# Kernel optimization log

Hardware: AMD Instinct MI355X
Metric: run time of the kernel (lower is better)

Reference implementation:

```python
import jax, jax.numpy as jnp
import numpy as np

N_CLASS = 100
HIDDEN = 768
BATCH = 512


def setup_inputs() -> dict:
    key = jax.random.key(0)
    kx, ky, km = jax.random.split(key, 3)
    x = jax.random.normal(kx, (BATCH, HIDDEN), dtype=jnp.float32)
    y = jax.random.randint(ky, (BATCH,), 0, N_CLASS, dtype=jnp.int64 if jax.config.jax_enable_x64 else jnp.int32)
    M = jax.random.normal(km, (N_CLASS, HIDDEN, HIDDEN), dtype=jnp.float32) * 0.1
    return {"x": x, "y": y, "M": M}


def _get_sym_M(M):
    # M: [n_class, H, H]
    h = M.shape[-1]
    Mt = jnp.triu(M)
    diag = Mt * jnp.eye(h, dtype=M.dtype)  # keeps only diagonal entries
    # detached ReLU correction: pushes near-zero/negative diagonal up by ~0.001
    Mt = Mt + jax.lax.stop_gradient(jax.nn.relu(-(diag - 0.001)))
    return jnp.einsum('chk,cjk->chj', Mt, Mt)  # Mt @ Mt^T, symmetric PSD


def reference(x, y, M):
    # Faithful to: one_hot(y) broadcast-select of sym_M then batched matvec.
    # Equivalent efficient form: gather selected class matrix, per-sample matvec.
    sym = _get_sym_M(M)            # [n_class, H, H]
    My = sym[y]                    # [B, H, H] gather (irregular access)
    return jnp.einsum('bh,bhk->bk', x, My)  # [B, H]
```

## Files before the change

### kernel.cpp

```cpp
#include <hip/hip_runtime.h>

#define NCLASS 100
#define HID    768
#define BATCH  512
#define SG     8
#define NPAN   12

__device__ __forceinline__ void build_list(const int* __restrict__ y, int c,
                                           int* slist, int* scnt, int t) {
    if (t < 64) {
        int n = 0;
        for (int r = 0; r < BATCH / 64; ++r) {
            const int b = r * 64 + t;
            const bool hit = (y[b] == c);
            const unsigned long long mask = __ballot(hit);
            if (hit) slist[n + __popcll(mask & ((1ull << t) - 1ull))] = b;
            n += __popcll(mask);
        }
        if (t == 0) *scnt = n;
    }
}

__global__ __launch_bounds__(256, 4) void kA(
    const float* __restrict__ x, const int* __restrict__ y,
    const float* __restrict__ M, float* __restrict__ T)
{
    const int c    = blockIdx.x;
    const int g    = (NPAN - 1) - blockIdx.y;
    const int t    = threadIdx.x;
    const int col0 = g * 64;

    __shared__ int   slist[BATCH];
    __shared__ int   scnt;
    __shared__ float xs[SG][HID];
    __shared__ float Xs[SG];
    __shared__ float red[4][16][4][SG + 1];
    __shared__ float dj_lds[64];

    build_list(y, c, slist, &scnt, t);
    __syncthreads();
    const int cnt = scnt;
    if (cnt == 0) return;

    const float* __restrict__ Mc   = M + (size_t)c * HID * HID;
    const float* __restrict__ Mpan = Mc + col0 + (t & 15) * 4;
    const int wv = t >> 6, ln = t & 63;
    const int hg = t >> 4, jq = t & 15;

    if (t < 64) {
        const int jg = col0 + t;
        dj_lds[t] = fmaxf(Mc[(size_t)jg * HID + jg], 1e-3f);
    }

    for (int g0 = 0; g0 < cnt; g0 += SG) {
        const int gs = min(SG, cnt - g0);
        __syncthreads();
        #pragma unroll
        for (int ss = 0; ss < 2; ++ss) {
            const int s = 2 * wv + ss;
            const int b = slist[g0 + (s < gs ? s : 0)];
            const float4* xr = (const float4*)(x + (size_t)b * HID);
            const float4 v0 = xr[ln], v1 = xr[ln + 64], v2 = xr[ln + 128];
            *(float4*)&xs[s][ln * 4]       = v0;
            *(float4*)&xs[s][ln * 4 + 256] = v1;
            *(float4*)&xs[s][ln * 4 + 512] = v2;
            float pX = ((v0.x + v0.y) + (v0.z + v0.w))
                     + ((v1.x + v1.y) + (v1.z + v1.w))
                     + ((v2.x + v2.y) + (v2.z + v2.w));
            #pragma unroll
            for (int off = 32; off; off >>= 1) pX += __shfl_xor(pX, off);
            if (ln == 0) Xs[s] = pX;
        }
        __syncthreads();

        float tp[4][SG];
        #pragma unroll
        for (int jj = 0; jj < 4; ++jj)
            #pragma unroll
            for (int s = 0; s < SG; ++s) tp[jj][s] = 0.f;

        int hb = 0;
        for (; hb + 128 <= col0; hb += 128) {
            float4 ma[4], mb[4];
            #pragma unroll
            for (int m = 0; m < 4; ++m)
                ma[m] = *(const float4*)(Mpan + (size_t)(hb + hg + 16 * m) * HID);
            #pragma unroll
            for (int m = 0; m < 4; ++m)
                mb[m] = *(const float4*)(Mpan + (size_t)(hb + 64 + hg + 16 * m) * HID);
            #pragma unroll
            for (int m = 0; m < 4; ++m) {
                const int h = hb + hg + 16 * m;
                #pragma unroll
                for (int s = 0; s < SG; ++s) {
                    const float xv = xs[s][h];
                    tp[0][s] = fmaf(xv, ma[m].x, tp[0][s]);
                    tp[1][s] = fmaf(xv, ma[m].y, tp[1][s]);
                    tp[2][s] = fmaf(xv, ma[m].z, tp[2][s]);
                    tp[3][s] = fmaf(xv, ma[m].w, tp[3][s]);
                }
            }
            #pragma unroll
            for (int m = 0; m < 4; ++m) {
                const int h = hb + 64 + hg + 16 * m;
                #pragma unroll
                for (int s = 0; s < SG; ++s) {
                    const float xv = xs[s][h];
                    tp[0][s] = fmaf(xv, mb[m].x, tp[0][s]);
                    tp[1][s] = fmaf(xv, mb[m].y, tp[1][s]);
                    tp[2][s] = fmaf(xv, mb[m].z, tp[2][s]);
                    tp[3][s] = fmaf(xv, mb[m].w, tp[3][s]);
                }
            }
        }
        if (hb < col0) {
            float4 ma[4];
            #pragma unroll
            for (int m = 0; m < 4; ++m)
                ma[m] = *(const float4*)(Mpan + (size_t)(hb + hg + 16 * m) * HID);
            #pragma unroll
            for (int m = 0; m < 4; ++m) {
                const int h = hb + hg + 16 * m;
                #pragma unroll
                for (int s = 0; s < SG; ++s) {
                    const float xv = xs[s][h];
                    tp[0][s] = fmaf(xv, ma[m].x, tp[0][s]);
                    tp[1][s] = fmaf(xv, ma[m].y, tp[1][s]);
                    tp[2][s] = fmaf(xv, ma[m].z, tp[2][s]);
                    tp[3][s] = fmaf(xv, ma[m].w, tp[3][s]);
                }
            }
        }
        {
            float4 ma[4];
            #pragma unroll
            for (int m = 0; m < 4; ++m) {
                const int hrel = hg + 16 * m;
                ma[m] = *(const float4*)(Mpan + (size_t)(col0 + hrel) * HID);
                if (4 * jq + 0 <= hrel) ma[m].x = 0.f;
                if (4 * jq + 1 <= hrel) ma[m].y = 0.f;
                if (4 * jq + 2 <= hrel) ma[m].z = 0.f;
                if (4 * jq + 3 <= hrel) ma[m].w = 0.f;
            }
            #pragma unroll
            for (int m = 0; m < 4; ++m) {
                const int h = col0 + hg + 16 * m;
                #pragma unroll
                for (int s = 0; s < SG; ++s) {
                    const float xv = xs[s][h];
                    tp[0][s] = fmaf(xv, ma[m].x, tp[0][s]);
                    tp[1][s] = fmaf(xv, ma[m].y, tp[1][s]);
                    tp[2][s] = fmaf(xv, ma[m].z, tp[2][s]);
                    tp[3][s] = fmaf(xv, ma[m].w, tp[3][s]);
                }
            }
        }
        #pragma unroll
        for (int m = 16; m <= 32; m <<= 1)
            #pragma unroll
            for (int jj = 0; jj < 4; ++jj)
                #pragma unroll
                for (int s = 0; s < SG; ++s)
                    tp[jj][s] += __shfl_xor(tp[jj][s], m);
        if (ln < 16) {
            #pragma unroll
            for (int jj = 0; jj < 4; ++jj)
                #pragma unroll
                for (int s = 0; s < SG; ++s)
                    red[wv][ln][jj][s] = tp[jj][s];
        }
        __syncthreads();
        {
            const int j = t & 63, jq2 = j >> 2, jj2 = j & 3;
            const int jg = col0 + j;
            #pragma unroll
            for (int ss = 0; ss < 2; ++ss) {
                const int s = (t >> 6) * 2 + ss;
                if (s < gs) {
                    const float u = (red[0][jq2][jj2][s] + red[1][jq2][jj2][s])
                                  + (red[2][jq2][jj2][s] + red[3][jq2][jj2][s]);
                    const float xj = xs[s][jg];
                    T[(size_t)slist[g0 + s] * HID + jg] =
                        u + dj_lds[j] * xj + 1e-3f * (Xs[s] - xj);
                }
            }
        }
    }
}

__global__ __launch_bounds__(256, 4) void kB(
    const int* __restrict__ y, const float* __restrict__ M,
    const float* __restrict__ T, float* __restrict__ out)
{
    const int c  = blockIdx.x;
    const int q  = blockIdx.y;
    const int t  = threadIdx.x;
    const int k0 = q * 64;

    __shared__ int   slist[BATCH];
    __shared__ int   scnt;
    __shared__ float ts[SG][HID];
    __shared__ float Tt[SG];
    __shared__ float ob[SG][64];
    __shared__ float dk_lds[64];

    build_list(y, c, slist, &scnt, t);
    __syncthreads();
    const int cnt = scnt;
    if (cnt == 0) return;

    const float* __restrict__ Mc = M + (size_t)c * HID * HID;
    const int wv = t >> 6, ln = t & 63;
    const int kr = t >> 4, cg = t & 15;
    const float* __restrict__ r0 = Mc + (size_t)(k0 + kr     ) * HID + k0 + cg * 4;
    const float* __restrict__ r1 = Mc + (size_t)(k0 + kr + 16) * HID + k0 + cg * 4;
    const float* __restrict__ r2 = Mc + (size_t)(k0 + kr + 32) * HID + k0 + cg * 4;
    const float* __restrict__ r3 = Mc + (size_t)(k0 + kr + 48) * HID + k0 + cg * 4;

    if (t < 64) {
        const int kg = k0 + t;
        dk_lds[t] = fmaxf(Mc[(size_t)kg * HID + kg], 1e-3f);
    }

    for (int g0 = 0; g0 < cnt; g0 += SG) {
        const int gs = min(SG, cnt - g0);
        __syncthreads();
        #pragma unroll
        for (int ss = 0; ss < 2; ++ss) {
            const int s = 2 * wv + ss;
            const int b = slist[g0 + (s < gs ? s : 0)];
            const float4* tr = (const float4*)(T + (size_t)b * HID);
            const float4 v0 = tr[ln], v1 = tr[ln + 64], v2 = tr[ln + 128];
            *(float4*)&ts[s][ln * 4]       = v0;
            *(float4*)&ts[s][ln * 4 + 256] = v1;
            *(float4*)&ts[s][ln * 4 + 512] = v2;
            float pT = ((v0.x + v0.y) + (v0.z + v0.w))
                     + ((v1.x + v1.y) + (v1.z + v1.w))
                     + ((v2.x + v2.y) + (v2.z + v2.w));
            #pragma unroll
            for (int off = 32; off; off >>= 1) pT += __shfl_xor(pT, off);
            if (ln == 0) Tt[s] = pT;
        }
        __syncthreads();

        float acc[4][SG];
        #pragma unroll
        for (int m = 0; m < 4; ++m)
            #pragma unroll
            for (int s = 0; s < SG; ++s) acc[m][s] = 0.f;

        {
            const int j0 = k0 + cg * 4;
            float4 mq[4];
            mq[0] = *(const float4*)(r0);
            mq[1] = *(const float4*)(r1);
            mq[2] = *(const float4*)(r2);
            mq[3] = *(const float4*)(r3);
            #pragma unroll
            for (int m = 0; m < 4; ++m) {
                const int k = k0 + 16 * m + kr;
                if (j0 + 0 <= k) mq[m].x = 0.f;
                if (j0 + 1 <= k) mq[m].y = 0.f;
                if (j0 + 2 <= k) mq[m].z = 0.f;
                if (j0 + 3 <= k) mq[m].w = 0.f;
            }
            #pragma unroll
            for (int s = 0; s < SG; ++s) {
                const float4 tv = *(const float4*)&ts[s][j0];
                #pragma unroll
                for (int m = 0; m < 4; ++m) {
                    acc[m][s] = fmaf(mq[m].x, tv.x, acc[m][s]);
                    acc[m][s] = fmaf(mq[m].y, tv.y, acc[m][s]);
                    acc[m][s] = fmaf(mq[m].z, tv.z, acc[m][s]);
                    acc[m][s] = fmaf(mq[m].w, tv.w, acc[m][s]);
                }
            }
        }
        int jb = k0 + 64;
        for (; jb + 128 <= HID; jb += 128) {
            float4 ma[4], mb[4];
            ma[0] = *(const float4*)(r0 + (jb - k0));
            ma[1] = *(const float4*)(r1 + (jb - k0));
            ma[2] = *(const float4*)(r2 + (jb - k0));
            ma[3] = *(const float4*)(r3 + (jb - k0));
            mb[0] = *(const float4*)(r0 + (jb - k0) + 64);
            mb[1] = *(const float4*)(r1 + (jb - k0) + 64);
            mb[2] = *(const float4*)(r2 + (jb - k0) + 64);
            mb[3] = *(const float4*)(r3 + (jb - k0) + 64);
            const int j0 = jb + cg * 4;
            #pragma unroll
            for (int s = 0; s < SG; ++s) {
                const float4 tv = *(const float4*)&ts[s][j0];
                #pragma unroll
                for (int m = 0; m < 4; ++m) {
                    acc[m][s] = fmaf(ma[m].x, tv.x, acc[m][s]);
                    acc[m][s] = fmaf(ma[m].y, tv.y, acc[m][s]);
                    acc[m][s] = fmaf(ma[m].z, tv.z, acc[m][s]);
                    acc[m][s] = fmaf(ma[m].w, tv.w, acc[m][s]);
                }
            }
            #pragma unroll
            for (int s = 0; s < SG; ++s) {
                const float4 tv = *(const float4*)&ts[s][j0 + 64];
                #pragma unroll
                for (int m = 0; m < 4; ++m) {
                    acc[m][s] = fmaf(mb[m].x, tv.x, acc[m][s]);
                    acc[m][s] = fmaf(mb[m].y, tv.y, acc[m][s]);
                    acc[m][s] = fmaf(mb[m].z, tv.z, acc[m][s]);
                    acc[m][s] = fmaf(mb[m].w, tv.w, acc[m][s]);
                }
            }
        }
        if (jb < HID) {
            float4 ma[4];
            ma[0] = *(const float4*)(r0 + (jb - k0));
            ma[1] = *(const float4*)(r1 + (jb - k0));
            ma[2] = *(const float4*)(r2 + (jb - k0));
            ma[3] = *(const float4*)(r3 + (jb - k0));
            const int j0 = jb + cg * 4;
            #pragma unroll
            for (int s = 0; s < SG; ++s) {
                const float4 tv = *(const float4*)&ts[s][j0];
                #pragma unroll
                for (int m = 0; m < 4; ++m) {
                    acc[m][s] = fmaf(ma[m].x, tv.x, acc[m][s]);
                    acc[m][s] = fmaf(ma[m].y, tv.y, acc[m][s]);
                    acc[m][s] = fmaf(ma[m].z, tv.z, acc[m][s]);
                    acc[m][s] = fmaf(ma[m].w, tv.w, acc[m][s]);
                }
            }
        }
        #pragma unroll
        for (int m2 = 1; m2 <= 8; m2 <<= 1)
            #pragma unroll
            for (int m = 0; m < 4; ++m)
                #pragma unroll
                for (int s = 0; s < SG; ++s)
                    acc[m][s] += __shfl_xor(acc[m][s], m2);
        if (cg == 0) {
            #pragma unroll
            for (int m = 0; m < 4; ++m)
                #pragma unroll
                for (int s = 0; s < SG; ++s)
                    ob[s][16 * m + kr] = acc[m][s];
        }
        __syncthreads();
        {
            const int j = t & 63;
            const int k = k0 + j;
            #pragma unroll
            for (int ss = 0; ss < 2; ++ss) {
                const int s = (t >> 6) * 2 + ss;
                if (s < gs) {
                    const float tk = ts[s][k];
                    out[(size_t)slist[g0 + s] * HID + k] =
                        ob[s][j] + dk_lds[j] * tk + 1e-3f * (Tt[s] - tk);
                }
            }
        }
    }
}

extern "C" void kernel_launch(void* const* d_in, const int* in_sizes, int n_in,
                              void* d_out, int out_size, void* d_ws, size_t ws_size,
                              hipStream_t stream) {
    const float* x = (const float*)d_in[0];
    const int*   y = (const int*)d_in[1];
    const float* M = (const float*)d_in[2];
    float* out = (float*)d_out;
    float* T   = (float*)d_ws;

    kA<<<dim3(NCLASS, NPAN), 256, 0, stream>>>(x, y, M, T);
    kB<<<dim3(NCLASS, NPAN), 256, 0, stream>>>(y, M, T, out);
}
```

Before: 90.98 us.

## Split triangular panels into balanced row chunks with partial sums and epilogue kernels

Each class's triangular work is split into 24 load-balanced tiles using lookup tables for panel and row-chunk indices, where the old code used 12 uneven column panels. Partial results go to workspace buffers and are combined by two new per-sample epilogue kernels, which also apply the diagonal and epsilon terms. The sample group size is doubled to 16 so each loaded M tile is reused across more samples. This adds two launches, extra workspace traffic and more register pressure, in exchange for better load balance and more parallelism.

```diff
diff --git a/kernel.cpp b/kernel.cpp
--- a/kernel.cpp
+++ b/kernel.cpp
@@ -3,8 +3,13 @@
 #define NCLASS 100
 #define HID    768
 #define BATCH  512
-#define SG     8
-#define NPAN   12
+#define SG     16
+#define BH     (BATCH * HID)
+
+__constant__ int gA_tab[24] = {3,4,5,6,7,7,8,8,9,9,10,10,11,11,11, 2,6,10, 1,5,9, 0,4,8};
+__constant__ int hA_tab[24] = {0,0,0,0,0,1,0,1,0,1, 0, 1, 0, 1, 2, 0,1, 2, 0,1,2, 0,1,2};
+__constant__ int qB_tab[24] = {0,0,1,1,2,2,3,3,4,5,6,7, 0,4,8, 1,5,9, 2,6,10, 3,7,11};
+__constant__ int vB_tab[24] = {1,2,1,2,1,2,1,2,2,2,2,2, 0,1,2, 0,1,2, 0, 1, 2, 0,1, 2};
 
 __device__ __forceinline__ void build_list(const int* __restrict__ y, int c,
                                            int* slist, int* scnt, int t) {
@@ -21,21 +26,22 @@
     }
 }
 
-__global__ __launch_bounds__(256, 4) void kA(
+__global__ __launch_bounds__(256, 3) void kA(
     const float* __restrict__ x, const int* __restrict__ y,
-    const float* __restrict__ M, float* __restrict__ T)
+    const float* __restrict__ M, float* __restrict__ Tp)
 {
+    const int t    = threadIdx.x;
     const int c    = blockIdx.x;
-    const int g    = (NPAN - 1) - blockIdx.y;
-    const int t    = threadIdx.x;
-    const int col0 = g * 64;
+    const int g    = gA_tab[blockIdx.y], h = hA_tab[blockIdx.y];
+    const int col0 = g * 64, row0 = h * 256;
+    const bool hasdiag = (h == (g >> 2));
+    const int rows = min(256, 64 * (g + 1) - row0);
+    const int bulk = hasdiag ? rows - 64 : rows;
 
     __shared__ int   slist[BATCH];
     __shared__ int   scnt;
-    __shared__ float xs[SG][HID];
-    __shared__ float Xs[SG];
+    __shared__ float xs[SG][256];
     __shared__ float red[4][16][4][SG + 1];
-    __shared__ float dj_lds[64];
 
     build_list(y, c, slist, &scnt, t);
     __syncthreads();
@@ -43,33 +49,22 @@
     if (cnt == 0) return;
 
     const float* __restrict__ Mc   = M + (size_t)c * HID * HID;
-    const float* __restrict__ Mpan = Mc + col0 + (t & 15) * 4;
-    const int wv = t >> 6, ln = t & 63;
-    const int hg = t >> 4, jq = t & 15;
-
-    if (t < 64) {
-        const int jg = col0 + t;
-        dj_lds[t] = fmaxf(Mc[(size_t)jg * HID + jg], 1e-3f);
-    }
+    const float* __restrict__ Mpan = Mc + (size_t)row0 * HID + col0 + (t & 15) * 4;
+    const int hg = t >> 4, jq = t & 15, wv = t >> 6, ln = t & 63;
 
     for (int g0 = 0; g0 < cnt; g0 += SG) {
         const int gs = min(SG, cnt - g0);
         __syncthreads();
-        #pragma unroll
-        for (int ss = 0; ss < 2; ++ss) {
-            const int s = 2 * wv + ss;
+        {
+            const int s = t >> 4, l = t & 15;
             const int b = slist[g0 + (s < gs ? s : 0)];
-            const float4* xr = (const float4*)(x + (size_t)b * HID);
-            const float4 v0 = xr[ln], v1 = xr[ln + 64], v2 = xr[ln + 128];
-            *(float4*)&xs[s][ln * 4]       = v0;
-            *(float4*)&xs[s][ln * 4 + 256] = v1;
-            *(float4*)&xs[s][ln * 4 + 512] = v2;
-            float pX = ((v0.x + v0.y) + (v0.z + v0.w))
-                     + ((v1.x + v1.y) + (v1.z + v1.w))
-                     + ((v2.x + v2.y) + (v2.z + v2.w));
-            #pragma unroll
-            for (int off = 32; off; off >>= 1) pX += __shfl_xor(pX, off);
-            if (ln == 0) Xs[s] = pX;
+            const float4* xr = (const float4*)(x + (size_t)b * HID + row0);
+            const float4 v0 = xr[l * 4], v1 = xr[l * 4 + 1],
+                         v2 = xr[l * 4 + 2], v3 = xr[l * 4 + 3];
+            *(float4*)&xs[s][l * 16]      = v0;
+            *(float4*)&xs[s][l * 16 + 4]  = v1;
+            *(float4*)&xs[s][l * 16 + 8]  = v2;
+            *(float4*)&xs[s][l * 16 + 12] = v3;
         }
         __syncthreads();
 
@@ -79,21 +74,21 @@
             #pragma unroll
             for (int s = 0; s < SG; ++s) tp[jj][s] = 0.f;
 
-        int hb = 0;
-        for (; hb + 128 <= col0; hb += 128) {
+        int r = 0;
+        for (; r + 128 <= bulk; r += 128) {
             float4 ma[4], mb[4];
             #pragma unroll
             for (int m = 0; m < 4; ++m)
-                ma[m] = *(const float4*)(Mpan + (size_t)(hb + hg + 16 * m) * HID);
-            #pragma unroll
-            for (int m = 0; m < 4; ++m)
-                mb[m] = *(const float4*)(Mpan + (size_t)(hb + 64 + hg + 16 * m) * HID);
+                ma[m] = *(const float4*)(Mpan + (size_t)(r + hg + 16 * m) * HID);
+            #pragma unroll
+            for (int m = 0; m < 4; ++m)
+                mb[m] = *(const float4*)(Mpan + (size_t)(r + 64 + hg + 16 * m) * HID);
             #pragma unroll
             for (int m = 0; m < 4; ++m) {
-                const int h = hb + hg + 16 * m;
+                const int lr = r + hg + 16 * m;
                 #pragma unroll
                 for (int s = 0; s < SG; ++s) {
-                    const float xv = xs[s][h];
+                    const float xv = xs[s][lr];
                     tp[0][s] = fmaf(xv, ma[m].x, tp[0][s]);
                     tp[1][s] = fmaf(xv, ma[m].y, tp[1][s]);
                     tp[2][s] = fmaf(xv, ma[m].z, tp[2][s]);
@@ -102,10 +97,10 @@
             }
             #pragma unroll
             for (int m = 0; m < 4; ++m) {
-                const int h = hb + 64 + hg + 16 * m;
+                const int lr = r + 64 + hg + 16 * m;
                 #pragma unroll
                 for (int s = 0; s < SG; ++s) {
-                    const float xv = xs[s][h];
+                    const float xv = xs[s][lr];
                     tp[0][s] = fmaf(xv, mb[m].x, tp[0][s]);
                     tp[1][s] = fmaf(xv, mb[m].y, tp[1][s]);
                     tp[2][s] = fmaf(xv, mb[m].z, tp[2][s]);
@@ -113,17 +108,17 @@
                 }
             }
         }
-        if (hb < col0) {
+        if (r < bulk) {
             float4 ma[4];
             #pragma unroll
             for (int m = 0; m < 4; ++m)
-                ma[m] = *(const float4*)(Mpan + (size_t)(hb + hg + 16 * m) * HID);
+                ma[m] = *(const float4*)(Mpan + (size_t)(r + hg + 16 * m) * HID);
             #pragma unroll
             for (int m = 0; m < 4; ++m) {
-                const int h = hb + hg + 16 * m;
+                const int lr = r + hg + 16 * m;
                 #pragma unroll
                 for (int s = 0; s < SG; ++s) {
-                    const float xv = xs[s][h];
+                    const float xv = xs[s][lr];
                     tp[0][s] = fmaf(xv, ma[m].x, tp[0][s]);
                     tp[1][s] = fmaf(xv, ma[m].y, tp[1][s]);
                     tp[2][s] = fmaf(xv, ma[m].z, tp[2][s]);
@@ -131,12 +126,12 @@
                 }
             }
         }
-        {
+        if (hasdiag) {
             float4 ma[4];
             #pragma unroll
             for (int m = 0; m < 4; ++m) {
                 const int hrel = hg + 16 * m;
-                ma[m] = *(const float4*)(Mpan + (size_t)(col0 + hrel) * HID);
+                ma[m] = *(const float4*)(Mpan + (size_t)(bulk + hrel) * HID);
                 if (4 * jq + 0 <= hrel) ma[m].x = 0.f;
                 if (4 * jq + 1 <= hrel) ma[m].y = 0.f;
                 if (4 * jq + 2 <= hrel) ma[m].z = 0.f;
@@ -144,10 +139,10 @@
             }
             #pragma unroll
             for (int m = 0; m < 4; ++m) {
-                const int h = col0 + hg + 16 * m;
+                const int lr = bulk + hg + 16 * m;
                 #pragma unroll
                 for (int s = 0; s < SG; ++s) {
-                    const float xv = xs[s][h];
+                    const float xv = xs[s][lr];
                     tp[0][s] = fmaf(xv, ma[m].x, tp[0][s]);
                     tp[1][s] = fmaf(xv, ma[m].y, tp[1][s]);
                     tp[2][s] = fmaf(xv, ma[m].z, tp[2][s]);
@@ -156,12 +151,12 @@
             }
         }
         #pragma unroll
-        for (int m = 16; m <= 32; m <<= 1)
+        for (int mm = 16; mm <= 32; mm <<= 1)
             #pragma unroll
             for (int jj = 0; jj < 4; ++jj)
                 #pragma unroll
                 for (int s = 0; s < SG; ++s)
-                    tp[jj][s] += __shfl_xor(tp[jj][s], m);
+                    tp[jj][s] += __shfl_xor(tp[jj][s], mm);
         if (ln < 16) {
             #pragma unroll
             for (int jj = 0; jj < 4; ++jj)
@@ -172,37 +167,68 @@
         __syncthreads();
         {
             const int j = t & 63, jq2 = j >> 2, jj2 = j & 3;
-            const int jg = col0 + j;
-            #pragma unroll
-            for (int ss = 0; ss < 2; ++ss) {
-                const int s = (t >> 6) * 2 + ss;
+            #pragma unroll
+            for (int ss = 0; ss < 4; ++ss) {
+                const int s = (t >> 6) * 4 + ss;
                 if (s < gs) {
                     const float u = (red[0][jq2][jj2][s] + red[1][jq2][jj2][s])
                                   + (red[2][jq2][jj2][s] + red[3][jq2][jj2][s]);
-                    const float xj = xs[s][jg];
-                    T[(size_t)slist[g0 + s] * HID + jg] =
-                        u + dj_lds[j] * xj + 1e-3f * (Xs[s] - xj);
+                    Tp[(size_t)h * BH + (size_t)slist[g0 + s] * HID + col0 + j] = u;
                 }
             }
         }
     }
 }
 
-__global__ __launch_bounds__(256, 4) void kB(
+__global__ __launch_bounds__(256) void kT(
+    const float* __restrict__ x, const int* __restrict__ y,
+    const float* __restrict__ M, const float* __restrict__ Tp,
+    float* __restrict__ T)
+{
+    const int b = blockIdx.x, t = threadIdx.x;
+    const int c = y[b];
+    __shared__ float wred[4];
+
+    const float* __restrict__ xb = x + (size_t)b * HID;
+    const float xv0 = xb[t], xv1 = xb[t + 256], xv2 = xb[t + 512];
+    float sx = xv0 + xv1 + xv2;
+    #pragma unroll
+    for (int off = 32; off; off >>= 1) sx += __shfl_xor(sx, off);
+    if ((t & 63) == 0) wred[t >> 6] = sx;
+    __syncthreads();
+    const float X = (wred[0] + wred[1]) + (wred[2] + wred[3]);
+
+    const float* __restrict__ Mc = M + (size_t)c * HID * HID;
+    const size_t bh = (size_t)b * HID;
+    const float u0 = Tp[bh + t];
+    const float u1 = Tp[bh + t + 256] + Tp[BH + bh + t + 256];
+    const float u2 = Tp[bh + t + 512] + Tp[BH + bh + t + 512] + Tp[2 * (size_t)BH + bh + t + 512];
+    const float uu[3] = {u0, u1, u2};
+    const float xx[3] = {xv0, xv1, xv2};
+    #pragma unroll
+    for (int qi = 0; qi < 3; ++qi) {
+        const int j = t + 256 * qi;
+        const float dj = fmaxf(Mc[(size_t)j * (HID + 1)], 1e-3f);
+        T[bh + j] = uu[qi] + dj * xx[qi] + 1e-3f * (X - xx[qi]);
+    }
+}
+
+__global__ __launch_bounds__(256, 3) void kB(
     const int* __restrict__ y, const float* __restrict__ M,
-    const float* __restrict__ T, float* __restrict__ out)
+    const float* __restrict__ T, float* __restrict__ P)
 {
+    const int t  = threadIdx.x;
     const int c  = blockIdx.x;
-    const int q  = blockIdx.y;
-    const int t  = threadIdx.x;
-    const int k0 = q * 64;
+    const int q  = qB_tab[blockIdx.y], v = vB_tab[blockIdx.y];
+    const int k0 = 64 * q;
+    const int c0 = max(256 * v, k0);
+    const int w  = 256 * (v + 1) - c0;
+    const bool hasdiag = (c0 == k0);
 
     __shared__ int   slist[BATCH];
     __shared__ int   scnt;
-    __shared__ float ts[SG][HID];
-    __shared__ float Tt[SG];
-    __shared__ float ob[SG][64];
-    __shared__ float dk_lds[64];
+    __shared__ float ts[SG][256];
+    __shared__ float ob[SG][65];
 
     build_list(y, c, slist, &scnt, t);
     __syncthreads();
@@ -210,36 +236,23 @@
     if (cnt == 0) return;
 
     const float* __restrict__ Mc = M + (size_t)c * HID * HID;
-    const int wv = t >> 6, ln = t & 63;
     const int kr = t >> 4, cg = t & 15;
-    const float* __restrict__ r0 = Mc + (size_t)(k0 + kr     ) * HID + k0 + cg * 4;
-    const float* __restrict__ r1 = Mc + (size_t)(k0 + kr + 16) * HID + k0 + cg * 4;
-    const float* __restrict__ r2 = Mc + (size_t)(k0 + kr + 32) * HID + k0 + cg * 4;
-    const float* __restrict__ r3 = Mc + (size_t)(k0 + kr + 48) * HID + k0 + cg * 4;
-
-    if (t < 64) {
-        const int kg = k0 + t;
-        dk_lds[t] = fmaxf(Mc[(size_t)kg * HID + kg], 1e-3f);
-    }
+    const float* __restrict__ Mrow = Mc + (size_t)(k0 + kr) * HID + c0 + cg * 4;
+    const int jl0 = (c0 - 256 * v) + cg * 4;
 
     for (int g0 = 0; g0 < cnt; g0 += SG) {
         const int gs = min(SG, cnt - g0);
         __syncthreads();
-        #pragma unroll
-        for (int ss = 0; ss < 2; ++ss) {
-            const int s = 2 * wv + ss;
+        {
+            const int s = t >> 4, l = t & 15;
             const int b = slist[g0 + (s < gs ? s : 0)];
-            const float4* tr = (const float4*)(T + (size_t)b * HID);
-            const float4 v0 = tr[ln], v1 = tr[ln + 64], v2 = tr[ln + 128];
-            *(float4*)&ts[s][ln * 4]       = v0;
-            *(float4*)&ts[s][ln * 4 + 256] = v1;
-            *(float4*)&ts[s][ln * 4 + 512] = v2;
-            float pT = ((v0.x + v0.y) + (v0.z + v0.w))
-                     + ((v1.x + v1.y) + (v1.z + v1.w))
-                     + ((v2.x + v2.y) + (v2.z + v2.w));
-            #pragma unroll
-            for (int off = 32; off; off >>= 1) pT += __shfl_xor(pT, off);
-            if (ln == 0) Tt[s] = pT;
+            const float4* tr = (const float4*)(T + (size_t)b * HID + 256 * v);
+            const float4 v0 = tr[l * 4], v1 = tr[l * 4 + 1],
+                         v2 = tr[l * 4 + 2], v3 = tr[l * 4 + 3];
+            *(float4*)&ts[s][l * 16]      = v0;
+            *(float4*)&ts[s][l * 16 + 4]  = v1;
+            *(float4*)&ts[s][l * 16 + 8]  = v2;
+            *(float4*)&ts[s][l * 16 + 12] = v3;
         }
         __syncthreads();
 
@@ -250,23 +263,23 @@
             for (int s = 0; s < SG; ++s) acc[m][s] = 0.f;
 
         {
-            const int j0 = k0 + cg * 4;
             float4 mq[4];
-            mq[0] = *(const float4*)(r0);
-            mq[1] = *(const float4*)(r1);
-            mq[2] = *(const float4*)(r2);
-            mq[3] = *(const float4*)(r3);
-            #pragma unroll
-            for (int m = 0; m < 4; ++m) {
-                const int k = k0 + 16 * m + kr;
-                if (j0 + 0 <= k) mq[m].x = 0.f;
-                if (j0 + 1 <= k) mq[m].y = 0.f;
-                if (j0 + 2 <= k) mq[m].z = 0.f;
-                if (j0 + 3 <= k) mq[m].w = 0.f;
+            #pragma unroll
+            for (int m = 0; m < 4; ++m)
+                mq[m] = *(const float4*)(Mrow + (size_t)(16 * m) * HID);
+            if (hasdiag) {
+                #pragma unroll
+                for (int m = 0; m < 4; ++m) {
+                    const int krel = kr + 16 * m;
+                    if (4 * cg + 0 <= krel) mq[m].x = 0.f;
+                    if (4 * cg + 1 <= krel) mq[m].y = 0.f;
+                    if (4 * cg + 2 <= krel) mq[m].z = 0.f;
+                    if (4 * cg + 3 <= krel) mq[m].w = 0.f;
+                }
             }
             #pragma unroll
             for (int s = 0; s < SG; ++s) {
-                const float4 tv = *(const float4*)&ts[s][j0];
+                const float4 tv = *(const float4*)&ts[s][jl0];
                 #pragma unroll
                 for (int m = 0; m < 4; ++m) {
                     acc[m][s] = fmaf(mq[m].x, tv.x, acc[m][s]);
@@ -276,21 +289,18 @@
                 }
             }
         }
-        int jb = k0 + 64;
-        for (; jb + 128 <= HID; jb += 128) {
+        int cb = 64;
+        for (; cb + 128 <= w; cb += 128) {
             float4 ma[4], mb[4];
-            ma[0] = *(const float4*)(r0 + (jb - k0));
-            ma[1] = *(const float4*)(r1 + (jb - k0));
-            ma[2] = *(const float4*)(r2 + (jb - k0));
-            ma[3] = *(const float4*)(r3 + (jb - k0));
-            mb[0] = *(const float4*)(r0 + (jb - k0) + 64);
-            mb[1] = *(const float4*)(r1 + (jb - k0) + 64);
-            mb[2] = *(const float4*)(r2 + (jb - k0) + 64);
-            mb[3] = *(const float4*)(r3 + (jb - k0) + 64);
-            const int j0 = jb + cg * 4;
+            #pragma unroll
+            for (int m = 0; m < 4; ++m)
+                ma[m] = *(const float4*)(Mrow + (size_t)(16 * m) * HID + cb);
+            #pragma unroll
+            for (int m = 0; m < 4; ++m)
+                mb[m] = *(const float4*)(Mrow + (size_t)(16 * m) * HID + cb + 64);
             #pragma unroll
             for (int s = 0; s < SG; ++s) {
-                const float4 tv = *(const float4*)&ts[s][j0];
+                const float4 tv = *(const float4*)&ts[s][jl0 + cb];
                 #pragma unroll
                 for (int m = 0; m < 4; ++m) {
                     acc[m][s] = fmaf(ma[m].x, tv.x, acc[m][s]);
@@ -301,7 +311,7 @@
             }
             #pragma unroll
             for (int s = 0; s < SG; ++s) {
-                const float4 tv = *(const float4*)&ts[s][j0 + 64];
+                const float4 tv = *(const float4*)&ts[s][jl0 + cb + 64];
                 #pragma unroll
                 for (int m = 0; m < 4; ++m) {
                     acc[m][s] = fmaf(mb[m].x, tv.x, acc[m][s]);
@@ -311,16 +321,14 @@
                 }
             }
         }
-        if (jb < HID) {
+        if (cb < w) {
             float4 ma[4];
-            ma[0] = *(const float4*)(r0 + (jb - k0));
-            ma[1] = *(const float4*)(r1 + (jb - k0));
-            ma[2] = *(const float4*)(r2 + (jb - k0));
-            ma[3] = *(const float4*)(r3 + (jb - k0));
-            const int j0 = jb + cg * 4;
+            #pragma unroll
+            for (int m = 0; m < 4; ++m)
+                ma[m] = *(const float4*)(Mrow + (size_t)(16 * m) * HID + cb);
             #pragma unroll
             for (int s = 0; s < SG; ++s) {
-                const float4 tv = *(const float4*)&ts[s][j0];
+                const float4 tv = *(const float4*)&ts[s][jl0 + cb];
                 #pragma unroll
                 for (int m = 0; m < 4; ++m) {
                     acc[m][s] = fmaf(ma[m].x, tv.x, acc[m][s]);
@@ -331,33 +339,61 @@
             }
         }
         #pragma unroll
-        for (int m2 = 1; m2 <= 8; m2 <<= 1)
+        for (int mm = 1; mm <= 8; mm <<= 1)
             #pragma unroll
             for (int m = 0; m < 4; ++m)
                 #pragma unroll
                 for (int s = 0; s < SG; ++s)
-                    acc[m][s] += __shfl_xor(acc[m][s], m2);
+                    acc[m][s] += __shfl_xor(acc[m][s], mm);
         if (cg == 0) {
             #pragma unroll
             for (int m = 0; m < 4; ++m)
                 #pragma unroll
                 for (int s = 0; s < SG; ++s)
-                    ob[s][16 * m + kr] = acc[m][s];
+                    ob[s][kr + 16 * m] = acc[m][s];
         }
         __syncthreads();
         {
             const int j = t & 63;
-            const int k = k0 + j;
-            #pragma unroll
-            for (int ss = 0; ss < 2; ++ss) {
-                const int s = (t >> 6) * 2 + ss;
-                if (s < gs) {
-                    const float tk = ts[s][k];
-                    out[(size_t)slist[g0 + s] * HID + k] =
-                        ob[s][j] + dk_lds[j] * tk + 1e-3f * (Tt[s] - tk);
-                }
-            }
-        }
+            #pragma unroll
+            for (int ss = 0; ss < 4; ++ss) {
+                const int s = (t >> 6) * 4 + ss;
+                if (s < gs)
+                    P[(size_t)v * BH + (size_t)slist[g0 + s] * HID + k0 + j] = ob[s][j];
+            }
+        }
+    }
+}
+
+__global__ __launch_bounds__(256) void k3(
+    const int* __restrict__ y, const float* __restrict__ M,
+    const float* __restrict__ T, const float* __restrict__ P,
+    float* __restrict__ out)
+{
+    const int b = blockIdx.x, t = threadIdx.x;
+    const int c = y[b];
+    __shared__ float wred[4];
+
+    const size_t bh = (size_t)b * HID;
+    const float t0 = T[bh + t], t1 = T[bh + t + 256], t2 = T[bh + t + 512];
+    float st = t0 + t1 + t2;
+    #pragma unroll
+    for (int off = 32; off; off >>= 1) st += __shfl_xor(st, off);
+    if ((t & 63) == 0) wred[t >> 6] = st;
+    __syncthreads();
+    const float Tt = (wred[0] + wred[1]) + (wred[2] + wred[3]);
+
+    const float* __restrict__ Mc = M + (size_t)c * HID * HID;
+    const float p0 = P[bh + t] + P[(size_t)BH + bh + t] + P[2 * (size_t)BH + bh + t];
+    const float p1 = P[(size_t)BH + bh + t + 256] + P[2 * (size_t)BH + bh + t + 256];
+    const float p2 = P[2 * (size_t)BH + bh + t + 512];
+    const float pp[3] = {p0, p1, p2};
+    const float tv[3] = {t0, t1, t2};
+    #pragma unroll
+    for (int qi = 0; qi < 3; ++qi) {
+        const int k = t + 256 * qi;
+        const float dk = fmaxf(Mc[(size_t)k * (HID + 1)], 1e-3f);
+        out[bh + k] = pp[qi] + dk * tv[qi] + 1e-3f * (Tt - tv[qi]);
     }
 }
 
@@ -368,8 +404,12 @@
     const int*   y = (const int*)d_in[1];
     const float* M = (const float*)d_in[2];
     float* out = (float*)d_out;
-    float* T   = (float*)d_ws;
-
-    kA<<<dim3(NCLASS, NPAN), 256, 0, stream>>>(x, y, M, T);
-    kB<<<dim3(NCLASS, NPAN), 256, 0, stream>>>(y, M, T, out);
-}
+    float* Tp  = (float*)d_ws;
+    float* T   = (float*)d_ws + 3 * (size_t)BH;
+    float* P   = (float*)d_ws + 4 * (size_t)BH;
+
+    kA<<<dim3(NCLASS, 24), 256, 0, stream>>>(x, y, M, Tp);
+    kT<<<dim3(BATCH), 256, 0, stream>>>(x, y, M, Tp, T);
+    kB<<<dim3(NCLASS, 24), 256, 0, stream>>>(y, M, T, P);
+    k3<<<dim3(BATCH), 256, 0, stream>>>(y, M, T, P, out);
+}
```

New measurement: 146.3 us. +60.8%, slower.

## Split triangular panel work across row chunks and precompute per-class lists and diagonals

Applied to the files above, without the earlier changes.

A new pre-kernel builds per-class sample lists, clamped diagonals and per-sample row sums once in global memory, instead of every block redoing the ballot scan and diagonal loads. kA now splits each column panel into 256-row chunks and dispatches 24 balanced work items per class through a constant table, evening out the triangular workload. Each chunk writes a partial T that kB adds up, and kB also applies the diagonal and epsilon correction while staging its input. The cost is an extra launch and extra global traffic for the partial-T buffers. It also assumes no class has more than 64 samples.

```diff
diff --git a/kernel.cpp b/kernel.cpp
--- a/kernel.cpp
+++ b/kernel.cpp
@@ -4,72 +4,86 @@
 #define HID    768
 #define BATCH  512
 #define SG     8
-#define NPAN   12
-
-__device__ __forceinline__ void build_list(const int* __restrict__ y, int c,
-                                           int* slist, int* scnt, int t) {
-    if (t < 64) {
-        int n = 0;
-        for (int r = 0; r < BATCH / 64; ++r) {
-            const int b = r * 64 + t;
-            const bool hit = (y[b] == c);
-            const unsigned long long mask = __ballot(hit);
-            if (hit) slist[n + __popcll(mask & ((1ull << t) - 1ull))] = b;
-            n += __popcll(mask);
-        }
-        if (t == 0) *scnt = n;
+#define BH     (BATCH * HID)
+
+__constant__ int gA_tab[24] = {3,4,5,6,7,7,8,8,9,9,10,10,11,11,11, 2,6,10, 1,5,9, 0,4,8};
+__constant__ int hA_tab[24] = {0,0,0,0,0,1,0,1,0,1, 0, 1, 0, 1, 2, 0,1, 2, 0,1,2, 0,1,2};
+
+__global__ __launch_bounds__(256) void k0(
+    const float* __restrict__ x, const int* __restrict__ y,
+    const float* __restrict__ M,
+    int* __restrict__ slist_g, int* __restrict__ scnt_g,
+    float* __restrict__ Xs_g, float* __restrict__ D_g)
+{
+    const int bb = blockIdx.x, t = threadIdx.x;
+    if (bb < NCLASS) {
+        const float* __restrict__ Mc = M + (size_t)bb * HID * HID;
+        #pragma unroll
+        for (int qi = 0; qi < 3; ++qi) {
+            const int j = t + 256 * qi;
+            D_g[bb * HID + j] = fmaxf(Mc[(size_t)j * (HID + 1)], 1e-3f);
+        }
+    } else if (bb == NCLASS) {
+        if (t < 64) {
+            for (int c = 0; c < NCLASS; ++c) {
+                int n = 0;
+                for (int r = 0; r < BATCH / 64; ++r) {
+                    const int b = r * 64 + t;
+                    const bool hit = (y[b] == c);
+                    const unsigned long long mask = __ballot(hit);
+                    if (hit) slist_g[c * 64 + n + __popcll(mask & ((1ull << t) - 1ull))] = b;
+                    n += __popcll(mask);
+                }
+                if (t == 0) scnt_g[c] = n;
+            }
+        }
+    } else {
+        const int s0 = (bb - NCLASS - 1) * 64;
+        const int sl = t >> 2, qq = t & 3;
+        const int b = s0 + sl;
+        const float4* __restrict__ xr = (const float4*)(x + (size_t)b * HID);
+        float p = 0.f;
+        for (int i = 0; i < 48; ++i) {
+            const float4 v = xr[qq * 48 + i];
+            p += (v.x + v.y) + (v.z + v.w);
+        }
+        p += __shfl_xor(p, 1);
+        p += __shfl_xor(p, 2);
+        if (qq == 0) Xs_g[b] = p;
     }
 }
 
-__global__ __launch_bounds__(256, 4) void kA(
-    const float* __restrict__ x, const int* __restrict__ y,
-    const float* __restrict__ M, float* __restrict__ T)
+__global__ __launch_bounds__(256, 5) void kA(
+    const float* __restrict__ x, const int* __restrict__ slist_g,
+    const int* __restrict__ scnt_g, const float* __restrict__ M,
+    float* __restrict__ Tp)
 {
+    const int t    = threadIdx.x;
     const int c    = blockIdx.x;
-    const int g    = (NPAN - 1) - blockIdx.y;
-    const int t    = threadIdx.x;
-    const int col0 = g * 64;
-
-    __shared__ int   slist[BATCH];
-    __shared__ int   scnt;
-    __shared__ float xs[SG][HID];
-    __shared__ float Xs[SG];
+    const int g    = gA_tab[blockIdx.y], h = hA_tab[blockIdx.y];
+    const int col0 = g * 64, row0 = h * 256;
+    const bool hasdiag = (h == (g >> 2));
+    const int rows = min(256, 64 * (g + 1) - row0);
+    const int bulk = hasdiag ? rows - 64 : rows;
+    const int cnt  = scnt_g[c];
+    if (cnt == 0) return;
+
+    __shared__ float xs[SG][256];
     __shared__ float red[4][16][4][SG + 1];
-    __shared__ float dj_lds[64];
-
-    build_list(y, c, slist, &scnt, t);
-    __syncthreads();
-    const int cnt = scnt;
-    if (cnt == 0) return;
 
     const float* __restrict__ Mc   = M + (size_t)c * HID * HID;
-    const float* __restrict__ Mpan = Mc + col0 + (t & 15) * 4;
-    const int wv = t >> 6, ln = t & 63;
-    const int hg = t >> 4, jq = t & 15;
-
-    if (t < 64) {
-        const int jg = col0 + t;
-        dj_lds[t] = fmaxf(Mc[(size_t)jg * HID + jg], 1e-3f);
-    }
+    const float* __restrict__ Mpan = Mc + (size_t)row0 * HID + col0 + (t & 15) * 4;
+    const int hg = t >> 4, jq = t & 15, wv = t >> 6, ln = t & 63;
 
     for (int g0 = 0; g0 < cnt; g0 += SG) {
         const int gs = min(SG, cnt - g0);
         __syncthreads();
-        #pragma unroll
-        for (int ss = 0; ss < 2; ++ss) {
-            const int s = 2 * wv + ss;
-            const int b = slist[g0 + (s < gs ? s : 0)];
-            const float4* xr = (const float4*)(x + (size_t)b * HID);
-            const float4 v0 = xr[ln], v1 = xr[ln + 64], v2 = xr[ln + 128];
-            *(float4*)&xs[s][ln * 4]       = v0;
-            *(float4*)&xs[s][ln * 4 + 256] = v1;
-            *(float4*)&xs[s][ln * 4 + 512] = v2;
-            float pX = ((v0.x + v0.y) + (v0.z + v0.w))
-                     + ((v1.x + v1.y) + (v1.z + v1.w))
-                     + ((v2.x + v2.y) + (v2.z + v2.w));
-            #pragma unroll
-            for (int off = 32; off; off >>= 1) pX += __shfl_xor(pX, off);
-            if (ln == 0) Xs[s] = pX;
+        {
+            const int s = t >> 5, l = t & 31;
+            const int b = slist_g[c * 64 + g0 + (s < gs ? s : 0)];
+            const float4* xr = (const float4*)(x + (size_t)b * HID + row0);
+            *(float4*)&xs[s][l * 8]     = xr[l * 2];
+            *(float4*)&xs[s][l * 8 + 4] = xr[l * 2 + 1];
         }
         __syncthreads();
 
@@ -79,51 +93,41 @@
             #pragma unroll
             for (int s = 0; s < SG; ++s) tp[jj][s] = 0.f;
 
-        int hb = 0;
-        for (; hb + 128 <= col0; hb += 128) {
-            float4 ma[4], mb[4];
+        for (int r = 0; r < bulk; r += 64) {
+            float4 ma[4];
             #pragma unroll
             for (int m = 0; m < 4; ++m)
-                ma[m] = *(const float4*)(Mpan + (size_t)(hb + hg + 16 * m) * HID);
-            #pragma unroll
-            for (int m = 0; m < 4; ++m)
-                mb[m] = *(const float4*)(Mpan + (size_t)(hb + 64 + hg + 16 * m) * HID);
+                ma[m] = *(const float4*)(Mpan + (size_t)(r + hg + 16 * m) * HID);
             #pragma unroll
             for (int m = 0; m < 4; ++m) {
-                const int h = hb + hg + 16 * m;
+                const int lr = r + hg + 16 * m;
                 #pragma unroll
                 for (int s = 0; s < SG; ++s) {
-                    const float xv = xs[s][h];
+                    const float xv = xs[s][lr];
                     tp[0][s] = fmaf(xv, ma[m].x, tp[0][s]);
                     tp[1][s] = fmaf(xv, ma[m].y, tp[1][s]);
                     tp[2][s] = fmaf(xv, ma[m].z, tp[2][s]);
                     tp[3][s] = fmaf(xv, ma[m].w, tp[3][s]);
                 }
             }
+        }
+        if (hasdiag) {
+            float4 ma[4];
             #pragma unroll
             for (int m = 0; m < 4; ++m) {
-                const int h = hb + 64 + hg + 16 * m;
+                const int hrel = hg + 16 * m;
+                ma[m] = *(const float4*)(Mpan + (size_t)(bulk + hrel) * HID);
+                if (4 * jq + 0 <= hrel) ma[m].x = 0.f;
+                if (4 * jq + 1 <= hrel) ma[m].y = 0.f;
+                if (4 * jq + 2 <= hrel) ma[m].z = 0.f;
+                if (4 * jq + 3 <= hrel) ma[m].w = 0.f;
+            }
+            #pragma unroll
+            for (int m = 0; m < 4; ++m) {
+                const int lr = bulk + hg + 16 * m;
                 #pragma unroll
                 for (int s = 0; s < SG; ++s) {
-                    const float xv = xs[s][h];
-                    tp[0][s] = fmaf(xv, mb[m].x, tp[0][s]);
-                    tp[1][s] = fmaf(xv, mb[m].y, tp[1][s]);
-                    tp[2][s] = fmaf(xv, mb[m].z, tp[2][s]);
-                    tp[3][s] = fmaf(xv, mb[m].w, tp[3][s]);
-                }
-            }
-        }
-        if (hb < col0) {
-            float4 ma[4];
-            #pragma unroll
-            for (int m = 0; m < 4; ++m)
-                ma[m] = *(const float4*)(Mpan + (size_t)(hb + hg + 16 * m) * HID);
-            #pragma unroll
-            for (int m = 0; m < 4; ++m) {
-                const int h = hb + hg + 16 * m;
-                #pragma unroll
-                for (int s = 0; s < SG; ++s) {
-                    const float xv = xs[s][h];
+                    const float xv = xs[s][lr];
                     tp[0][s] = fmaf(xv, ma[m].x, tp[0][s]);
                     tp[1][s] = fmaf(xv, ma[m].y, tp[1][s]);
                     tp[2][s] = fmaf(xv, ma[m].z, tp[2][s]);
@@ -131,37 +135,13 @@
                 }
             }
         }
-        {
-            float4 ma[4];
-            #pragma unroll
-            for (int m = 0; m < 4; ++m) {
-                const int hrel = hg + 16 * m;
-                ma[m] = *(const float4*)(Mpan + (size_t)(col0 + hrel) * HID);
-                if (4 * jq + 0 <= hrel) ma[m].x = 0.f;
-                if (4 * jq + 1 <= hrel) ma[m].y = 0.f;
-                if (4 * jq + 2 <= hrel) ma[m].z = 0.f;
-                if (4 * jq + 3 <= hrel) ma[m].w = 0.f;
-            }
-            #pragma unroll
-            for (int m = 0; m < 4; ++m) {
-                const int h = col0 + hg + 16 * m;
-                #pragma unroll
-                for (int s = 0; s < SG; ++s) {
-                    const float xv = xs[s][h];
-                    tp[0][s] = fmaf(xv, ma[m].x, tp[0][s]);
-                    tp[1][s] = fmaf(xv, ma[m].y, tp[1][s]);
-                    tp[2][s] = fmaf(xv, ma[m].z, tp[2][s]);
-                    tp[3][s] = fmaf(xv, ma[m].w, tp[3][s]);
-                }
-            }
-        }
-        #pragma unroll
-        for (int m = 16; m <= 32; m <<= 1)
+        #pragma unroll
+        for (int mm = 16; mm <= 32; mm <<= 1)
             #pragma unroll
             for (int jj = 0; jj < 4; ++jj)
                 #pragma unroll
                 for (int s = 0; s < SG; ++s)
-                    tp[jj][s] += __shfl_xor(tp[jj][s], m);
+                    tp[jj][s] += __shfl_xor(tp[jj][s], mm);
         if (ln < 16) {
             #pragma unroll
             for (int jj = 0; jj < 4; ++jj)
@@ -172,16 +152,13 @@
         __syncthreads();
         {
             const int j = t & 63, jq2 = j >> 2, jj2 = j & 3;
-            const int jg = col0 + j;
             #pragma unroll
             for (int ss = 0; ss < 2; ++ss) {
                 const int s = (t >> 6) * 2 + ss;
                 if (s < gs) {
                     const float u = (red[0][jq2][jj2][s] + red[1][jq2][jj2][s])
                                   + (red[2][jq2][jj2][s] + red[3][jq2][jj2][s]);
-                    const float xj = xs[s][jg];
-                    T[(size_t)slist[g0 + s] * HID + jg] =
-                        u + dj_lds[j] * xj + 1e-3f * (Xs[s] - xj);
+                    Tp[(size_t)h * BH + (size_t)slist_g[c * 64 + g0 + s] * HID + col0 + j] = u;
                 }
             }
         }
@@ -189,57 +166,73 @@
 }
 
 __global__ __launch_bounds__(256, 4) void kB(
-    const int* __restrict__ y, const float* __restrict__ M,
-    const float* __restrict__ T, float* __restrict__ out)
+    const float* __restrict__ x, const int* __restrict__ slist_g,
+    const int* __restrict__ scnt_g, const float* __restrict__ M,
+    const float* __restrict__ Tp, const float* __restrict__ Xs_g,
+    const float* __restrict__ D_g, float* __restrict__ out)
 {
+    const int t  = threadIdx.x;
     const int c  = blockIdx.x;
     const int q  = blockIdx.y;
-    const int t  = threadIdx.x;
     const int k0 = q * 64;
-
-    __shared__ int   slist[BATCH];
-    __shared__ int   scnt;
+    const int cnt = scnt_g[c];
+    if (cnt == 0) return;
+
     __shared__ float ts[SG][HID];
+    __shared__ float dl[HID];
     __shared__ float Tt[SG];
-    __shared__ float ob[SG][64];
-    __shared__ float dk_lds[64];
-
-    build_list(y, c, slist, &scnt, t);
-    __syncthreads();
-    const int cnt = scnt;
-    if (cnt == 0) return;
+    __shared__ float ob[SG][65];
+
+    if (t < 192) *(float4*)&dl[t * 4] = ((const float4*)(D_g + c * HID))[t];
 
     const float* __restrict__ Mc = M + (size_t)c * HID * HID;
-    const int wv = t >> 6, ln = t & 63;
     const int kr = t >> 4, cg = t & 15;
     const float* __restrict__ r0 = Mc + (size_t)(k0 + kr     ) * HID + k0 + cg * 4;
     const float* __restrict__ r1 = Mc + (size_t)(k0 + kr + 16) * HID + k0 + cg * 4;
     const float* __restrict__ r2 = Mc + (size_t)(k0 + kr + 32) * HID + k0 + cg * 4;
     const float* __restrict__ r3 = Mc + (size_t)(k0 + kr + 48) * HID + k0 + cg * 4;
 
-    if (t < 64) {
-        const int kg = k0 + t;
-        dk_lds[t] = fmaxf(Mc[(size_t)kg * HID + kg], 1e-3f);
-    }
-
     for (int g0 = 0; g0 < cnt; g0 += SG) {
         const int gs = min(SG, cnt - g0);
         __syncthreads();
-        #pragma unroll
-        for (int ss = 0; ss < 2; ++ss) {
-            const int s = 2 * wv + ss;
-            const int b = slist[g0 + (s < gs ? s : 0)];
-            const float4* tr = (const float4*)(T + (size_t)b * HID);
-            const float4 v0 = tr[ln], v1 = tr[ln + 64], v2 = tr[ln + 128];
-            *(float4*)&ts[s][ln * 4]       = v0;
-            *(float4*)&ts[s][ln * 4 + 256] = v1;
-            *(float4*)&ts[s][ln * 4 + 512] = v2;
-            float pT = ((v0.x + v0.y) + (v0.z + v0.w))
-                     + ((v1.x + v1.y) + (v1.z + v1.w))
-                     + ((v2.x + v2.y) + (v2.z + v2.w));
-            #pragma unroll
-            for (int off = 32; off; off >>= 1) pT += __shfl_xor(pT, off);
-            if (ln == 0) Tt[s] = pT;
+        {
+            const int s = t >> 5, l = t & 31;
+            const int b = slist_g[c * 64 + g0 + (s < gs ? s : 0)];
+            const size_t bh4 = (size_t)b * (HID / 4);
+            const float4* __restrict__ x4 = (const float4*)x;
+            const float4* __restrict__ T0 = (const float4*)Tp;
+            const float4* __restrict__ T1 = (const float4*)(Tp + (size_t)BH);
+            const float4* __restrict__ T2 = (const float4*)(Tp + 2 * (size_t)BH);
+            const float Xb = Xs_g[b];
+            float psum = 0.f;
+            #pragma unroll
+            for (int r = 0; r < 3; ++r) {
+                #pragma unroll
+                for (int u = 0; u < 2; ++u) {
+                    const int j4 = r * 64 + l * 2 + u;
+                    float4 tv = T0[bh4 + j4];
+                    if (r >= 1) {
+                        const float4 a = T1[bh4 + j4];
+                        tv.x += a.x; tv.y += a.y; tv.z += a.z; tv.w += a.w;
+                    }
+                    if (r >= 2) {
+                        const float4 a = T2[bh4 + j4];
+                        tv.x += a.x; tv.y += a.y; tv.z += a.z; tv.w += a.w;
+                    }
+                    const float4 xv = x4[bh4 + j4];
+                    const float4 dv = *(const float4*)&dl[j4 * 4];
+                    float4 o;
+                    o.x = tv.x + dv.x * xv.x + 1e-3f * (Xb - xv.x);
+                    o.y = tv.y + dv.y * xv.y + 1e-3f * (Xb - xv.y);
+                    o.z = tv.z + dv.z * xv.z + 1e-3f * (Xb - xv.z);
+                    o.w = tv.w + dv.w * xv.w + 1e-3f * (Xb - xv.w);
+                    *(float4*)&ts[s][j4 * 4] = o;
+                    psum += (o.x + o.y) + (o.z + o.w);
+                }
+            }
+            #pragma unroll
+            for (int off = 1; off <= 16; off <<= 1) psum += __shfl_xor(psum, off);
+            if (l == 0) Tt[s] = psum;
         }
         __syncthreads();
 
@@ -331,12 +324,12 @@
             }
         }
         #pragma unroll
-        for (int m2 = 1; m2 <= 8; m2 <<= 1)
+        for (int mm = 1; mm <= 8; mm <<= 1)
             #pragma unroll
             for (int m = 0; m < 4; ++m)
                 #pragma unroll
                 for (int s = 0; s < SG; ++s)
-                    acc[m][s] += __shfl_xor(acc[m][s], m2);
+                    acc[m][s] += __shfl_xor(acc[m][s], mm);
         if (cg == 0) {
             #pragma unroll
             for (int m = 0; m < 4; ++m)
@@ -353,8 +346,8 @@
                 const int s = (t >> 6) * 2 + ss;
                 if (s < gs) {
                     const float tk = ts[s][k];
-                    out[(size_t)slist[g0 + s] * HID + k] =
-                        ob[s][j] + dk_lds[j] * tk + 1e-3f * (Tt[s] - tk);
+                    out[(size_t)slist_g[c * 64 + g0 + s] * HID + k] =
+                        ob[s][j] + dl[k] * tk + 1e-3f * (Tt[s] - tk);
                 }
             }
         }
@@ -368,8 +361,14 @@
     const int*   y = (const int*)d_in[1];
     const float* M = (const float*)d_in[2];
     float* out = (float*)d_out;
-    float* T   = (float*)d_ws;
-
-    kA<<<dim3(NCLASS, NPAN), 256, 0, stream>>>(x, y, M, T);
-    kB<<<dim3(NCLASS, NPAN), 256, 0, stream>>>(y, M, T, out);
+
+    float* Tp      = (float*)d_ws;
+    int*   slist_g = (int*)((float*)d_ws + 3 * (size_t)BH);
+    int*   scnt_g  = slist_g + NCLASS * 64;
+    float* Xs_g    = (float*)(scnt_g + 128);
+    float* D_g     = Xs_g + BATCH;
+
+    k0<<<dim3(NCLASS + 1 + BATCH / 64), 256, 0, stream>>>(x, y, M, slist_g, scnt_g, Xs_g, D_g);
+    kA<<<dim3(NCLASS, 24), 256, 0, stream>>>(x, slist_g, scnt_g, M, Tp);
+    kB<<<dim3(NCLASS, 12), 256, 0, stream>>>(x, slist_g, scnt_g, M, Tp, Xs_g, D_g, out);
 }
```

New measurement: 120.7 us. +32.7%, slower.

## Precompute per-class sample lists in a separate kernel and reorder grid

Applied to the files above, without the earlier changes.

The per-class sample-list construction moves out of kA and kB into a small new kernel, k0, which writes the lists and counts to workspace. This removes the redundant list building that every block repeated, and drops slist from shared memory. The grid is also transposed so the panel index varies fastest, so neighbouring blocks share one class matrix in cache, and the padding on the reduction buffer is removed. The cost is an extra kernel launch, global reads of the list inside the loops, and possible LDS bank conflicts now that the padding is gone.

```diff
diff --git a/kernel.cpp b/kernel.cpp
--- a/kernel.cpp
+++ b/kernel.cpp
@@ -6,41 +6,38 @@
 #define SG     8
 #define NPAN   12
 
-__device__ __forceinline__ void build_list(const int* __restrict__ y, int c,
-                                           int* slist, int* scnt, int t) {
-    if (t < 64) {
-        int n = 0;
-        for (int r = 0; r < BATCH / 64; ++r) {
-            const int b = r * 64 + t;
-            const bool hit = (y[b] == c);
-            const unsigned long long mask = __ballot(hit);
-            if (hit) slist[n + __popcll(mask & ((1ull << t) - 1ull))] = b;
-            n += __popcll(mask);
-        }
-        if (t == 0) *scnt = n;
-    }
+__global__ __launch_bounds__(64) void k0(
+    const int* __restrict__ y, int* __restrict__ slist_g,
+    int* __restrict__ scnt_g)
+{
+    const int c = blockIdx.x, t = threadIdx.x;
+    int n = 0;
+    for (int r = 0; r < BATCH / 64; ++r) {
+        const int b = r * 64 + t;
+        const bool hit = (y[b] == c);
+        const unsigned long long mask = __ballot(hit);
+        if (hit) slist_g[c * 512 + n + __popcll(mask & ((1ull << t) - 1ull))] = b;
+        n += __popcll(mask);
+    }
+    if (t == 0) scnt_g[c] = n;
 }
 
 __global__ __launch_bounds__(256, 4) void kA(
-    const float* __restrict__ x, const int* __restrict__ y,
-    const float* __restrict__ M, float* __restrict__ T)
+    const float* __restrict__ x, const int* __restrict__ slist_g,
+    const int* __restrict__ scnt_g, const float* __restrict__ M,
+    float* __restrict__ T)
 {
-    const int c    = blockIdx.x;
-    const int g    = (NPAN - 1) - blockIdx.y;
+    const int c    = blockIdx.y;
+    const int g    = (NPAN - 1) - blockIdx.x;
     const int t    = threadIdx.x;
     const int col0 = g * 64;
-
-    __shared__ int   slist[BATCH];
-    __shared__ int   scnt;
+    const int cnt  = scnt_g[c];
+    if (cnt == 0) return;
+
     __shared__ float xs[SG][HID];
     __shared__ float Xs[SG];
-    __shared__ float red[4][16][4][SG + 1];
+    __shared__ float red[4][16][4][SG];
     __shared__ float dj_lds[64];
-
-    build_list(y, c, slist, &scnt, t);
-    __syncthreads();
-    const int cnt = scnt;
-    if (cnt == 0) return;
 
     const float* __restrict__ Mc   = M + (size_t)c * HID * HID;
     const float* __restrict__ Mpan = Mc + col0 + (t & 15) * 4;
@@ -58,7 +55,7 @@
         #pragma unroll
         for (int ss = 0; ss < 2; ++ss) {
             const int s = 2 * wv + ss;
-            const int b = slist[g0 + (s < gs ? s : 0)];
+            const int b = slist_g[c * 512 + g0 + (s < gs ? s : 0)];
             const float4* xr = (const float4*)(x + (size_t)b * HID);
             const float4 v0 = xr[ln], v1 = xr[ln + 64], v2 = xr[ln + 128];
             *(float4*)&xs[s][ln * 4]       = v0;
@@ -180,7 +177,7 @@
                     const float u = (red[0][jq2][jj2][s] + red[1][jq2][jj2][s])
                                   + (red[2][jq2][jj2][s] + red[3][jq2][jj2][s]);
                     const float xj = xs[s][jg];
-                    T[(size_t)slist[g0 + s] * HID + jg] =
+                    T[(size_t)slist_g[c * 512 + g0 + s] * HID + jg] =
                         u + dj_lds[j] * xj + 1e-3f * (Xs[s] - xj);
                 }
             }
@@ -189,25 +186,21 @@
 }
 
 __global__ __launch_bounds__(256, 4) void kB(
-    const int* __restrict__ y, const float* __restrict__ M,
-    const float* __restrict__ T, float* __restrict__ out)
+    const int* __restrict__ slist_g, const int* __restrict__ scnt_g,
+    const float* __restrict__ M, const float* __restrict__ T,
+    float* __restrict__ out)
 {
-    const int c  = blockIdx.x;
-    const int q  = blockIdx.y;
+    const int c  = blockIdx.y;
+    const int q  = blockIdx.x;
     const int t  = threadIdx.x;
     const int k0 = q * 64;
-
-    __shared__ int   slist[BATCH];
-    __shared__ int   scnt;
+    const int cnt = scnt_g[c];
+    if (cnt == 0) return;
+
     __shared__ float ts[SG][HID];
     __shared__ float Tt[SG];
     __shared__ float ob[SG][64];
     __shared__ float dk_lds[64];
-
-    build_list(y, c, slist, &scnt, t);
-    __syncthreads();
-    const int cnt = scnt;
-    if (cnt == 0) return;
 
     const float* __restrict__ Mc = M + (size_t)c * HID * HID;
     const int wv = t >> 6, ln = t & 63;
@@ -228,7 +221,7 @@
         #pragma unroll
         for (int ss = 0; ss < 2; ++ss) {
             const int s = 2 * wv + ss;
-            const int b = slist[g0 + (s < gs ? s : 0)];
+            const int b = slist_g[c * 512 + g0 + (s < gs ? s : 0)];
             const float4* tr = (const float4*)(T + (size_t)b * HID);
             const float4 v0 = tr[ln], v1 = tr[ln + 64], v2 = tr[ln + 128];
             *(float4*)&ts[s][ln * 4]       = v0;
@@ -353,7 +346,7 @@
                 const int s = (t >> 6) * 2 + ss;
                 if (s < gs) {
                     const float tk = ts[s][k];
-                    out[(size_t)slist[g0 + s] * HID + k] =
+                    out[(size_t)slist_g[c * 512 + g0 + s] * HID + k] =
                         ob[s][j] + dk_lds[j] * tk + 1e-3f * (Tt[s] - tk);
                 }
             }
@@ -368,8 +361,12 @@
     const int*   y = (const int*)d_in[1];
     const float* M = (const float*)d_in[2];
     float* out = (float*)d_out;
-    float* T   = (float*)d_ws;
-
-    kA<<<dim3(NCLASS, NPAN), 256, 0, stream>>>(x, y, M, T);
-    kB<<<dim3(NCLASS, NPAN), 256, 0, stream>>>(y, M, T, out);
+
+    float* T       = (float*)d_ws;
+    int*   slist_g = (int*)((float*)d_ws + BATCH * HID);
+    int*   scnt_g  = slist_g + NCLASS * 512;
+
+    k0<<<dim3(NCLASS), 64, 0, stream>>>(y, slist_g, scnt_g);
+    kA<<<dim3(NPAN, NCLASS), 256, 0, stream>>>(x, slist_g, scnt_g, M, T);
+    kB<<<dim3(NPAN, NCLASS), 256, 0, stream>>>(slist_g, scnt_g, M, T, out);
 }
```

New measurement: 105.8 us. +16.3%, slower.
